# Kernel tuning notes

Hardware: AMD Instinct MI355X
Metric: run time of the kernel (lower is better)

## Reference

```python
import jax, jax.numpy as jnp
import numpy as np

D_MODEL = 512
N_HEADS = 8
D_K = D_MODEL // N_HEADS
WINDOW = 32  # attention restricted to |i-j| <= WINDOW//2
SCALE = float(np.sqrt(D_K))


def setup_inputs() -> dict:
    key = jax.random.key(0)
    ks = jax.random.split(key, 11)
    B, S, D = 2, 4096, D_MODEL
    inv = 1.0 / np.sqrt(D)
    inp = {
        "query": jax.random.normal(ks[0], (B, S, D), jnp.float32),
        "key": jax.random.normal(ks[1], (B, S, D), jnp.float32),
        "value": jax.random.normal(ks[2], (B, S, D), jnp.float32),
        # torch nn.Linear params: weight (out,in), bias (out,)
        "wq": jax.random.uniform(ks[3], (D, D), jnp.float32, -inv, inv),
        "bq": jax.random.uniform(ks[4], (D,), jnp.float32, -inv, inv),
        "wk": jax.random.uniform(ks[5], (D, D), jnp.float32, -inv, inv),
        "bk": jax.random.uniform(ks[6], (D,), jnp.float32, -inv, inv),
        "wv": jax.random.uniform(ks[7], (D, D), jnp.float32, -inv, inv),
        "bv": jax.random.uniform(ks[8], (D,), jnp.float32, -inv, inv),
        "wo": jax.random.uniform(ks[9], (D, D), jnp.float32, -inv, inv),
        "bo": jax.random.uniform(ks[10], (D,), jnp.float32, -inv, inv),
    }
    return inp


def _linear(x, w, b):
    # torch: y = x @ w.T + b
    return jnp.einsum('bsd,od->bso', x, w) + b


def reference(query, key, value, wq, bq, wk, bk, wv, bv, wo, bo):
    B, S, D = query.shape
    # project and split heads -> [B, H, S, d_k]
    def split(x):
        return x.reshape(B, S, N_HEADS, D_K).transpose(0, 2, 1, 3)
    Q = split(_linear(query, wq, bq))
    K = split(_linear(key, wk, bk))
    V = split(_linear(value, wv, bv))
    # full scores then banded mask (faithful to original dense-masked impl)
    scores = jnp.einsum('bhqd,bhkd->bhqk', Q, K) / SCALE
    i = jnp.arange(S)[:, None]
    j = jnp.arange(S)[None, :]
    band = jnp.abs(i - j) <= (WINDOW // 2)  # [S, S]
    scores = jnp.where(band[None, None, :, :], scores, -1e9)
    attn = jax.nn.softmax(scores, axis=-1)
    ctx = jnp.einsum('bhqk,bhkd->bhqd', attn, V)
    ctx = ctx.transpose(0, 2, 1, 3).reshape(B, S, D)
    return _linear(ctx, wo, bo)
```

## Files before the change

kernel.cpp:

```cpp
#include <hip/hip_runtime.h>
#include <hip/hip_bf16.h>

using u16 = unsigned short;
using u32 = unsigned int;

typedef float f32x4 __attribute__((ext_vector_type(4)));
typedef __bf16 bf16x8 __attribute__((ext_vector_type(8)));

constexpr int B_ = 2;
constexpr int S_ = 4096;
constexpr int D_ = 512;
constexpr int H_ = 8;
constexpr int DK_ = 64;
constexpr int M_ = B_ * S_;
constexpr int K_ = 512;

__device__ __forceinline__ float bf2f(u16 u) {
  return __uint_as_float(((u32)u) << 16);
}
__device__ __forceinline__ u16 f2bf(float x) {
  u32 u = __float_as_uint(x);
  u = (u + 0x7fffu + ((u >> 16) & 1u)) >> 16;
  return (u16)u;
}
__device__ __forceinline__ u32 pack2(float a, float b) {
  return (u32)f2bf(a) | ((u32)f2bf(b) << 16);
}
__device__ __forceinline__ u32 cvtpk(float a, float b) {
  u32 r;
  asm("v_cvt_pk_bf16_f32 %0, %1, %2" : "=v"(r) : "v"(a), "v"(b));
  return r;
}

__device__ __forceinline__ void gload16(const void* g, void* l) {
  __builtin_amdgcn_global_load_lds((const __attribute__((address_space(1))) void*)g,
                                   (__attribute__((address_space(3))) void*)l,
                                   16, 0, 0);
}

constexpr int NG_W = 4 * (262144 / 8);

__global__ __launch_bounds__(256) void convert_w(
    const float* __restrict__ wq, const float* __restrict__ wk,
    const float* __restrict__ wv, const float* __restrict__ wo,
    u16* __restrict__ wqb, u16* __restrict__ wkb, u16* __restrict__ wvb,
    u16* __restrict__ wob)
{
  const int g8 = blockIdx.x * 256 + threadIdx.x;
  if (g8 >= NG_W) return;
  const int t = g8 >> 15;
  const int r = g8 & 32767;
  const float* s = (t == 0) ? wq : (t == 1) ? wk : (t == 2) ? wv : wo;
  u16* d = (t == 0) ? wqb : (t == 1) ? wkb : (t == 2) ? wvb : wob;
  const size_t off = (size_t)r * 8;
  const float4 x = *(const float4*)(s + off);
  const float4 y = *(const float4*)(s + off + 4);
  uint4 o;
  o.x = pack2(x.x, x.y); o.y = pack2(x.z, x.w);
  o.z = pack2(y.x, y.y); o.w = pack2(y.z, y.w);
  *(uint4*)(d + off) = o;
}

template<int MODE>
__device__ __forceinline__ void gemm_qkv_body(const float* __restrict__ A,
                                              const u16* __restrict__ Wt,
                                              const float* __restrict__ bias,
                                              void* __restrict__ Cout,
                                              u16* __restrict__ As,
                                              u16* __restrict__ Bs2)
{
  const int tid  = threadIdx.x;
  const int lane = tid & 63;
  const int w    = tid >> 6;
  const int wm   = w >> 1;
  const int wn   = w & 1;
  const int m0   = blockIdx.x * 128;
  const int n0   = blockIdx.y * 128;
  const int qr   = lane & 15;
  const int g    = lane >> 4;

  const int sr8 = tid >> 3;
  const int c8  = tid & 7;
  const float* afp = A + (size_t)(m0 + sr8) * K_ + c8 * 8;
  char* awr = (char*)As + sr8 * 128 + ((c8 ^ (sr8 & 7)) * 16);

  float4 ax_[4], ay_[4];
  auto a_issue = [&](int t) {
#pragma unroll
    for (int p = 0; p < 4; ++p) {
      const float* s = afp + t * 64 + (size_t)(p * 32) * K_;
      ax_[p] = *(const float4*)s;
      ay_[p] = *(const float4*)(s + 4);
    }
  };
  auto a_write = [&]() {
#pragma unroll
    for (int p = 0; p < 4; ++p) {
      uint4 o;
      o.x = cvtpk(ax_[p].x, ax_[p].y);
      o.y = cvtpk(ax_[p].z, ax_[p].w);
      o.z = cvtpk(ay_[p].x, ay_[p].y);
      o.w = cvtpk(ay_[p].z, ay_[p].w);
      *(uint4*)(awr + p * 32 * 128) = o;
    }
  };

  const int swz8 = ((lane & 7) ^ (lane >> 3)) * 8;
  const u16* b0 = Wt + (size_t)(n0 + w * 32 + (lane >> 3)) * K_ + swz8;
  auto stage_B = [&](int t, int buf) {
    u16* dst = Bs2 + buf * (128 * 64) + (w * 32) * 64;
#pragma unroll
    for (int p = 0; p < 4; ++p)
      gload16(b0 + t * 64 + (size_t)p * 8 * K_, dst + (p * 8) * 64);
  };

  f32x4 acc[4][4] = {};

  a_issue(0);
  stage_B(0, 0);
  a_write();
  __syncthreads();

  const int axr = (qr & 7) << 4;
  const char* ab = (const char*)As + (wm * 64 + qr) * 128;

  constexpr int NT = K_ / 64;
#pragma unroll 1
  for (int t = 0; t < NT; ++t) {
    const int buf = t & 1;
    if (t + 1 < NT) {
      a_issue(t + 1);
      stage_B(t + 1, buf ^ 1);
    }

    const char* bb = (const char*)(Bs2 + buf * (128 * 64)) + (wn * 64 + qr) * 128;
#pragma unroll
    for (int kk = 0; kk < 2; ++kk) {
      bf16x8 af[4], bfr[4];
#pragma unroll
      for (int i = 0; i < 4; ++i)
        af[i]  = *(const bf16x8*)(ab + i * 2048 + ((g * 16 + kk * 64) ^ axr));
#pragma unroll
      for (int j = 0; j < 4; ++j)
        bfr[j] = *(const bf16x8*)(bb + j * 2048 + ((g * 16 + kk * 64) ^ axr));
#pragma unroll
      for (int i = 0; i < 4; ++i)
#pragma unroll
        for (int j = 0; j < 4; ++j)
          acc[i][j] = __builtin_amdgcn_mfma_f32_16x16x32_bf16(af[i], bfr[j], acc[i][j], 0, 0, 0);
    }

    if (t + 1 < NT) {
      __syncthreads();
      a_write();
      __syncthreads();
    }
  }

#pragma unroll
  for (int j = 0; j < 4; ++j) {
    const int col = n0 + wn * 64 + j * 16 + qr;
    const float bv = bias[col];
#pragma unroll
    for (int i = 0; i < 4; ++i) {
      const int rbase = m0 + wm * 64 + i * 16 + g * 4;
      if constexpr (MODE == 2) {
        const int bb2 = rbase >> 12;
        const int ss = rbase & (S_ - 1);
        const int hh = col >> 6;
        const int dd = col & (DK_ - 1);
        uint2 pk;
        pk.x = pack2(acc[i][j][0] + bv, acc[i][j][1] + bv);
        pk.y = pack2(acc[i][j][2] + bv, acc[i][j][3] + bv);
        *(uint2*)&((u16*)Cout)[((size_t)((bb2 * H_ + hh) * DK_ + dd)) * S_ + ss] = pk;
      } else {
#pragma unroll
        for (int r = 0; r < 4; ++r)
          ((u16*)Cout)[(size_t)(rbase + r) * D_ + col] = f2bf(acc[i][j][r] + bv);
      }
    }
  }
}

__global__ __launch_bounds__(256, 3) void gemm_qkv(
    const float* __restrict__ q, const float* __restrict__ k, const float* __restrict__ v,
    const u16* __restrict__ wqb, const u16* __restrict__ wkb, const u16* __restrict__ wvb,
    const float* __restrict__ bq, const float* __restrict__ bk, const float* __restrict__ bv,
    u16* __restrict__ Qo, u16* __restrict__ Ko, u16* __restrict__ Vo)
{
  __shared__ u16 As[128 * 64];
  __shared__ u16 Bs2[2][128 * 64];
  if (blockIdx.z == 0)      gemm_qkv_body<0>(q, wqb, bq, Qo, As, &Bs2[0][0]);
  else if (blockIdx.z == 1) gemm_qkv_body<0>(k, wkb, bk, Ko, As, &Bs2[0][0]);
  else                      gemm_qkv_body<2>(v, wvb, bv, Vo, As, &Bs2[0][0]);
}

__global__ __launch_bounds__(256, 2) void gemm_out(
    const u16* __restrict__ A, const u16* __restrict__ Wt,
    const float* __restrict__ bias, float* __restrict__ C)
{
  __shared__ u16 As2[2][64 * 64];
  __shared__ u16 Bs2[2][128 * 64];

  const int tid  = threadIdx.x;
  const int lane = tid & 63;
  const int w    = tid >> 6;
  const int wm   = w >> 1;
  const int wn   = w & 1;
  const int m0   = blockIdx.x * 64;
  const int n0   = blockIdx.y * 128;
  const int qr   = lane & 15;
  const int g    = lane >> 4;

  const int swz8 = ((lane & 7) ^ (lane >> 3)) * 8;
  const u16* a0 = A  + (size_t)(m0 + w * 16 + (lane >> 3)) * K_ + swz8;
  const u16* b0 = Wt + (size_t)(n0 + w * 32 + (lane >> 3)) * K_ + swz8;

  auto stage = [&](int t, int buf) {
#pragma unroll
    for (int p = 0; p < 2; ++p)
      gload16(a0 + t * 64 + (size_t)p * 8 * K_, &As2[buf][(w * 16 + p * 8) * 64]);
#pragma unroll
    for (int p = 0; p < 4; ++p)
      gload16(b0 + t * 64 + (size_t)p * 8 * K_, &Bs2[buf][(w * 32 + p * 8) * 64]);
  };

  f32x4 acc[2][4] = {};
  stage(0, 0);
  __syncthreads();

  const int ax = (qr & 7) << 4;

  constexpr int NT = K_ / 64;
#pragma unroll 1
  for (int t = 0; t < NT; ++t) {
    const int buf = t & 1;
    if (t + 1 < NT) stage(t + 1, buf ^ 1);

    const char* ab = (const char*)&As2[buf][0] + (wm * 32 + qr) * 128;
    const char* bb = (const char*)&Bs2[buf][0] + (wn * 64 + qr) * 128;
#pragma unroll
    for (int kk = 0; kk < 2; ++kk) {
      bf16x8 af[2], bfr[4];
#pragma unroll
      for (int i = 0; i < 2; ++i)
        af[i]  = *(const bf16x8*)(ab + i * 2048 + ((g * 16 + kk * 64) ^ ax));
#pragma unroll
      for (int j = 0; j < 4; ++j)
        bfr[j] = *(const bf16x8*)(bb + j * 2048 + ((g * 16 + kk * 64) ^ ax));
#pragma unroll
      for (int i = 0; i < 2; ++i)
#pragma unroll
        for (int j = 0; j < 4; ++j)
          acc[i][j] = __builtin_amdgcn_mfma_f32_16x16x32_bf16(af[i], bfr[j], acc[i][j], 0, 0, 0);
    }
    if (t + 1 < NT) __syncthreads();
  }

#pragma unroll
  for (int j = 0; j < 4; ++j) {
    const int col = n0 + wn * 64 + j * 16 + qr;
    const float bv = bias[col];
#pragma unroll
    for (int i = 0; i < 2; ++i) {
      const int rbase = m0 + wm * 32 + i * 16 + g * 4;
#pragma unroll
      for (int r = 0; r < 4; ++r)
        C[(size_t)(rbase + r) * D_ + col] = acc[i][j][r] + bv;
    }
  }
}

__global__ __launch_bounds__(256) void attn_band_mfma(
    const u16* __restrict__ Q, const u16* __restrict__ K,
    const u16* __restrict__ Vt, u16* __restrict__ Ctx)
{
  constexpr int LDP = 72;
  __shared__ u16 P_lds[4][16 * LDP];

  const int lane = threadIdx.x & 63;
  const int w    = threadIdx.x >> 6;
  const int wid  = blockIdx.x * 4 + w;
  const int q0   = (wid & 255) << 4;
  const int bh   = wid >> 8;
  const int bb   = bh >> 3;
  const int hh   = bh & (H_ - 1);

  u16* pl = &P_lds[w][0];
  const int qr = lane & 15;
  const int g  = lane >> 4;

  *(uint2*)&pl[qr * LDP + 48 + 4 * g] = make_uint2(0u, 0u);

  bf16x8 qf[2];
  {
    const u16* qp = Q + ((size_t)(bb * S_ + q0 + qr)) * D_ + hh * DK_ + 8 * g;
    qf[0] = *(const bf16x8*)qp;
    qf[1] = *(const bf16x8*)(qp + 32);
  }

  f32x4 sc[3];
#pragma unroll
  for (int t = 0; t < 3; ++t) {
    int j = q0 - 16 + 16 * t + qr;
    j = min(max(j, 0), S_ - 1);
    const u16* kp = K + ((size_t)(bb * S_ + j)) * D_ + hh * DK_ + 8 * g;
    const bf16x8 kf0 = *(const bf16x8*)kp;
    const bf16x8 kf1 = *(const bf16x8*)(kp + 32);
    f32x4 a = {};
    a = __builtin_amdgcn_mfma_f32_16x16x32_bf16(kf0, qf[0], a, 0, 0, 0);
    a = __builtin_amdgcn_mfma_f32_16x16x32_bf16(kf1, qf[1], a, 0, 0, 0);
    sc[t] = a;
  }

  float s[3][4];
  float mx = -INFINITY;
#pragma unroll
  for (int t = 0; t < 3; ++t)
#pragma unroll
    for (int r = 0; r < 4; ++r) {
      const int joff = 16 * t + 4 * g + r;
      const int j = q0 - 16 + joff;
      const bool ok = (joff >= qr) && (joff <= qr + 32) && (j >= 0) && (j < S_);
      const float v = ok ? sc[t][r] * 0.125f : -INFINITY;
      s[t][r] = v;
      mx = fmaxf(mx, v);
    }
  mx = fmaxf(mx, __shfl_xor(mx, 16));
  mx = fmaxf(mx, __shfl_xor(mx, 32));

  float p[3][4];
  float den = 0.f;
#pragma unroll
  for (int t = 0; t < 3; ++t)
#pragma unroll
    for (int r = 0; r < 4; ++r) {
      p[t][r] = __expf(s[t][r] - mx);
      den += p[t][r];
    }
  den += __shfl_xor(den, 16);
  den += __shfl_xor(den, 32);
  const float inv = 1.0f / den;

#pragma unroll
  for (int t = 0; t < 3; ++t) {
    uint2 pk;
    pk.x = pack2(p[t][0] * inv, p[t][1] * inv);
    pk.y = pack2(p[t][2] * inv, p[t][3] * inv);
    *(uint2*)&pl[qr * LDP + 16 * t + 4 * g] = pk;
  }

  f32x4 cacc[4] = {};
#pragma unroll
  for (int jc = 0; jc < 2; ++jc) {
    const bf16x8 pa = *(const bf16x8*)&pl[qr * LDP + 8 * g + 32 * jc];
#pragma unroll
    for (int nt = 0; nt < 4; ++nt) {
      int jj = q0 - 16 + 8 * g + 32 * jc;
      jj = min(max(jj, 0), S_ - 8);
      const u16* vp = Vt + ((size_t)bh * DK_ + 16 * nt + qr) * S_ + jj;
      const bf16x8 vf = *(const bf16x8*)vp;
      cacc[nt] = __builtin_amdgcn_mfma_f32_16x16x32_bf16(pa, vf, cacc[nt], 0, 0, 0);
    }
  }

#pragma unroll
  for (int nt = 0; nt < 4; ++nt)
#pragma unroll
    for (int r = 0; r < 4; ++r) {
      const int qq = 4 * g + r;
      const int dd = 16 * nt + qr;
      Ctx[((size_t)(bb * S_ + q0 + qq)) * D_ + hh * DK_ + dd] = f2bf(cacc[nt][r]);
    }
}

extern "C" void kernel_launch(void* const* d_in, const int* in_sizes, int n_in,
                              void* d_out, int out_size, void* d_ws, size_t ws_size,
                              hipStream_t stream)
{
  const float* query = (const float*)d_in[0];
  const float* key   = (const float*)d_in[1];
  const float* value = (const float*)d_in[2];
  const float* wq    = (const float*)d_in[3];
  const float* bq    = (const float*)d_in[4];
  const float* wk    = (const float*)d_in[5];
  const float* bk    = (const float*)d_in[6];
  const float* wv    = (const float*)d_in[7];
  const float* bv    = (const float*)d_in[8];
  const float* wo    = (const float*)d_in[9];
  const float* bo    = (const float*)d_in[10];

  const size_t seg = (size_t)M_ * D_;
  u16* Qw  = (u16*)d_ws;
  u16* Kw  = Qw + seg;
  u16* Vw  = Kw + seg;
  u16* Cw  = Vw + seg;
  u16* wqb = Cw + seg;
  u16* wkb = wqb + (size_t)D_ * D_;
  u16* wvb = wkb + (size_t)D_ * D_;
  u16* wob = wvb + (size_t)D_ * D_;

  dim3 blk(256);
  convert_w<<<dim3((NG_W + 255) / 256), blk, 0, stream>>>(
      wq, wk, wv, wo, wqb, wkb, wvb, wob);
  gemm_qkv<<<dim3(M_ / 128, D_ / 128, 3), blk, 0, stream>>>(
      query, key, value, wqb, wkb, wvb, bq, bk, bv, Qw, Kw, Vw);
  attn_band_mfma<<<dim3((B_ * H_ * S_) / 64), blk, 0, stream>>>(Qw, Kw, Vw, Cw);
  gemm_out<<<dim3(M_ / 64, D_ / 128), blk, 0, stream>>>(Cw, wob, bo, (float*)d_out);
}
```

Baseline: 55.11 us.

## Fuse weight bf16 conversion into QKV GEMM and attention kernels, drop convert kernel

Removes the separate weight-conversion kernel launch. The QKV GEMM now loads fp32 weights and converts them to bf16 in registers before writing to LDS, and the output-projection weight conversion is folded into the attention kernel's prologue. This saves a launch and a pass over the weights, but doubles weight bytes read per GEMM block, adds conversion ALU work and registers, and replaces the async double-buffered B staging with synchronous single-buffer staging.

```diff
diff --git a/kernel.cpp b/kernel.cpp
--- a/kernel.cpp
+++ b/kernel.cpp
@@ -38,36 +38,13 @@
                                    16, 0, 0);
 }
 
-constexpr int NG_W = 4 * (262144 / 8);
-
-__global__ __launch_bounds__(256) void convert_w(
-    const float* __restrict__ wq, const float* __restrict__ wk,
-    const float* __restrict__ wv, const float* __restrict__ wo,
-    u16* __restrict__ wqb, u16* __restrict__ wkb, u16* __restrict__ wvb,
-    u16* __restrict__ wob)
-{
-  const int g8 = blockIdx.x * 256 + threadIdx.x;
-  if (g8 >= NG_W) return;
-  const int t = g8 >> 15;
-  const int r = g8 & 32767;
-  const float* s = (t == 0) ? wq : (t == 1) ? wk : (t == 2) ? wv : wo;
-  u16* d = (t == 0) ? wqb : (t == 1) ? wkb : (t == 2) ? wvb : wob;
-  const size_t off = (size_t)r * 8;
-  const float4 x = *(const float4*)(s + off);
-  const float4 y = *(const float4*)(s + off + 4);
-  uint4 o;
-  o.x = pack2(x.x, x.y); o.y = pack2(x.z, x.w);
-  o.z = pack2(y.x, y.y); o.w = pack2(y.z, y.w);
-  *(uint4*)(d + off) = o;
-}
-
 template<int MODE>
 __device__ __forceinline__ void gemm_qkv_body(const float* __restrict__ A,
-                                              const u16* __restrict__ Wt,
+                                              const float* __restrict__ W,
                                               const float* __restrict__ bias,
                                               void* __restrict__ Cout,
                                               u16* __restrict__ As,
-                                              u16* __restrict__ Bs2)
+                                              u16* __restrict__ Bs)
 {
   const int tid  = threadIdx.x;
   const int lane = tid & 63;
@@ -81,16 +58,28 @@
 
   const int sr8 = tid >> 3;
   const int c8  = tid & 7;
+  const int swb = (c8 ^ (sr8 & 7)) * 16;
+
   const float* afp = A + (size_t)(m0 + sr8) * K_ + c8 * 8;
-  char* awr = (char*)As + sr8 * 128 + ((c8 ^ (sr8 & 7)) * 16);
-
-  float4 ax_[4], ay_[4];
+  const float* wfp = W + (size_t)(n0 + sr8) * K_ + c8 * 8;
+  char* awr = (char*)As + sr8 * 128 + swb;
+  char* bwr = (char*)Bs + sr8 * 128 + swb;
+
+  float4 ax_[4], ay_[4], bx_[4], by_[4];
   auto a_issue = [&](int t) {
 #pragma unroll
     for (int p = 0; p < 4; ++p) {
       const float* s = afp + t * 64 + (size_t)(p * 32) * K_;
       ax_[p] = *(const float4*)s;
       ay_[p] = *(const float4*)(s + 4);
+    }
+  };
+  auto b_issue = [&](int t) {
+#pragma unroll
+    for (int p = 0; p < 4; ++p) {
+      const float* s = wfp + t * 64 + (size_t)(p * 32) * K_;
+      bx_[p] = *(const float4*)s;
+      by_[p] = *(const float4*)(s + 4);
     }
   };
   auto a_write = [&]() {
@@ -104,36 +93,36 @@
       *(uint4*)(awr + p * 32 * 128) = o;
     }
   };
-
-  const int swz8 = ((lane & 7) ^ (lane >> 3)) * 8;
-  const u16* b0 = Wt + (size_t)(n0 + w * 32 + (lane >> 3)) * K_ + swz8;
-  auto stage_B = [&](int t, int buf) {
-    u16* dst = Bs2 + buf * (128 * 64) + (w * 32) * 64;
-#pragma unroll
-    for (int p = 0; p < 4; ++p)
-      gload16(b0 + t * 64 + (size_t)p * 8 * K_, dst + (p * 8) * 64);
+  auto b_write = [&]() {
+#pragma unroll
+    for (int p = 0; p < 4; ++p) {
+      uint4 o;
+      o.x = cvtpk(bx_[p].x, bx_[p].y);
+      o.y = cvtpk(bx_[p].z, bx_[p].w);
+      o.z = cvtpk(by_[p].x, by_[p].y);
+      o.w = cvtpk(by_[p].z, by_[p].w);
+      *(uint4*)(bwr + p * 32 * 128) = o;
+    }
   };
 
   f32x4 acc[4][4] = {};
 
-  a_issue(0);
-  stage_B(0, 0);
-  a_write();
+  a_issue(0); b_issue(0);
+  a_write(); b_write();
   __syncthreads();
 
   const int axr = (qr & 7) << 4;
   const char* ab = (const char*)As + (wm * 64 + qr) * 128;
+  const char* bb = (const char*)Bs + (wn * 64 + qr) * 128;
 
   constexpr int NT = K_ / 64;
 #pragma unroll 1
   for (int t = 0; t < NT; ++t) {
-    const int buf = t & 1;
     if (t + 1 < NT) {
       a_issue(t + 1);
-      stage_B(t + 1, buf ^ 1);
-    }
-
-    const char* bb = (const char*)(Bs2 + buf * (128 * 64)) + (wn * 64 + qr) * 128;
+      b_issue(t + 1);
+    }
+
 #pragma unroll
     for (int kk = 0; kk < 2; ++kk) {
       bf16x8 af[4], bfr[4];
@@ -153,6 +142,7 @@
     if (t + 1 < NT) {
       __syncthreads();
       a_write();
+      b_write();
       __syncthreads();
     }
   }
@@ -184,15 +174,15 @@
 
 __global__ __launch_bounds__(256, 3) void gemm_qkv(
     const float* __restrict__ q, const float* __restrict__ k, const float* __restrict__ v,
-    const u16* __restrict__ wqb, const u16* __restrict__ wkb, const u16* __restrict__ wvb,
+    const float* __restrict__ wq, const float* __restrict__ wk, const float* __restrict__ wv,
     const float* __restrict__ bq, const float* __restrict__ bk, const float* __restrict__ bv,
     u16* __restrict__ Qo, u16* __restrict__ Ko, u16* __restrict__ Vo)
 {
   __shared__ u16 As[128 * 64];
-  __shared__ u16 Bs2[2][128 * 64];
-  if (blockIdx.z == 0)      gemm_qkv_body<0>(q, wqb, bq, Qo, As, &Bs2[0][0]);
-  else if (blockIdx.z == 1) gemm_qkv_body<0>(k, wkb, bk, Ko, As, &Bs2[0][0]);
-  else                      gemm_qkv_body<2>(v, wvb, bv, Vo, As, &Bs2[0][0]);
+  __shared__ u16 Bs[128 * 64];
+  if (blockIdx.z == 0)      gemm_qkv_body<0>(q, wq, bq, Qo, As, Bs);
+  else if (blockIdx.z == 1) gemm_qkv_body<0>(k, wk, bk, Ko, As, Bs);
+  else                      gemm_qkv_body<2>(v, wv, bv, Vo, As, Bs);
 }
 
 __global__ __launch_bounds__(256, 2) void gemm_out(
@@ -273,8 +263,14 @@
 
 __global__ __launch_bounds__(256) void attn_band_mfma(
     const u16* __restrict__ Q, const u16* __restrict__ K,
-    const u16* __restrict__ Vt, u16* __restrict__ Ctx)
+    const u16* __restrict__ Vt, u16* __restrict__ Ctx,
+    const float* __restrict__ wo, u16* __restrict__ wob)
 {
+  {
+    const int idx = blockIdx.x * 256 + threadIdx.x;
+    wob[idx] = f2bf(wo[idx]);
+  }
+
   constexpr int LDP = 72;
   __shared__ u16 P_lds[4][16 * LDP];
 
@@ -395,16 +391,12 @@
   u16* Kw  = Qw + seg;
   u16* Vw  = Kw + seg;
   u16* Cw  = Vw + seg;
-  u16* wqb = Cw + seg;
-  u16* wkb = wqb + (size_t)D_ * D_;
-  u16* wvb = wkb + (size_t)D_ * D_;
-  u16* wob = wvb + (size_t)D_ * D_;
+  u16* wob = Cw + seg;
 
   dim3 blk(256);
-  convert_w<<<dim3((NG_W + 255) / 256), blk, 0, stream>>>(
-      wq, wk, wv, wo, wqb, wkb, wvb, wob);
   gemm_qkv<<<dim3(M_ / 128, D_ / 128, 3), blk, 0, stream>>>(
-      query, key, value, wqb, wkb, wvb, bq, bk, bv, Qw, Kw, Vw);
-  attn_band_mfma<<<dim3((B_ * H_ * S_) / 64), blk, 0, stream>>>(Qw, Kw, Vw, Cw);
+      query, key, value, wq, wk, wv, bq, bk, bv, Qw, Kw, Vw);
+  attn_band_mfma<<<dim3((B_ * H_ * S_) / 64), blk, 0, stream>>>(
+      Qw, Kw, Vw, Cw, wo, wob);
   gemm_out<<<dim3(M_ / 64, D_ / 128), blk, 0, stream>>>(Cw, wob, bo, (float*)d_out);
 }
```

New measurement: 56.26 us. 2.1% more time.

## Load QKV A-operand directly into MFMA registers; shrink out-proj tile to 32 rows

Applied to the files above, without the earlier changes.

The QKV projection GEMM now reads fp32 activations straight from global memory into the per-lane MFMA fragment layout and converts them to bf16 in registers. This removes the A-tile LDS staging buffer and one barrier per k-step. The cost is uncoalesced, redundant global reads, since each of the two wn warps loads the same A rows. The output GEMM drops from 64-row to 32-row tiles with 4 warps split along N and launch bounds raised to 4 blocks per CU, doubling the grid for better occupancy at lower per-warp MFMA reuse.

```diff
diff --git a/kernel.cpp b/kernel.cpp
--- a/kernel.cpp
+++ b/kernel.cpp
@@ -66,7 +66,6 @@
                                               const u16* __restrict__ Wt,
                                               const float* __restrict__ bias,
                                               void* __restrict__ Cout,
-                                              u16* __restrict__ As,
                                               u16* __restrict__ Bs2)
 {
   const int tid  = threadIdx.x;
@@ -79,30 +78,32 @@
   const int qr   = lane & 15;
   const int g    = lane >> 4;
 
-  const int sr8 = tid >> 3;
-  const int c8  = tid & 7;
-  const float* afp = A + (size_t)(m0 + sr8) * K_ + c8 * 8;
-  char* awr = (char*)As + sr8 * 128 + ((c8 ^ (sr8 & 7)) * 16);
-
-  float4 ax_[4], ay_[4];
+  const float* arow = A + (size_t)(m0 + wm * 64 + qr) * K_ + 8 * g;
+
+  float4 palo[4][2], pahi[4][2];
   auto a_issue = [&](int t) {
 #pragma unroll
-    for (int p = 0; p < 4; ++p) {
-      const float* s = afp + t * 64 + (size_t)(p * 32) * K_;
-      ax_[p] = *(const float4*)s;
-      ay_[p] = *(const float4*)(s + 4);
-    }
+    for (int i = 0; i < 4; ++i)
+#pragma unroll
+      for (int kk = 0; kk < 2; ++kk) {
+        const float* s = arow + (size_t)(i * 16) * K_ + t * 64 + kk * 32;
+        palo[i][kk] = *(const float4*)s;
+        pahi[i][kk] = *(const float4*)(s + 4);
+      }
   };
-  auto a_write = [&]() {
-#pragma unroll
-    for (int p = 0; p < 4; ++p) {
-      uint4 o;
-      o.x = cvtpk(ax_[p].x, ax_[p].y);
-      o.y = cvtpk(ax_[p].z, ax_[p].w);
-      o.z = cvtpk(ay_[p].x, ay_[p].y);
-      o.w = cvtpk(ay_[p].z, ay_[p].w);
-      *(uint4*)(awr + p * 32 * 128) = o;
-    }
+  bf16x8 af[4][2];
+  auto a_cvt = [&]() {
+#pragma unroll
+    for (int i = 0; i < 4; ++i)
+#pragma unroll
+      for (int kk = 0; kk < 2; ++kk) {
+        union { u32 u[4]; bf16x8 v; } u;
+        u.u[0] = cvtpk(palo[i][kk].x, palo[i][kk].y);
+        u.u[1] = cvtpk(palo[i][kk].z, palo[i][kk].w);
+        u.u[2] = cvtpk(pahi[i][kk].x, pahi[i][kk].y);
+        u.u[3] = cvtpk(pahi[i][kk].z, pahi[i][kk].w);
+        af[i][kk] = u.v;
+      }
   };
 
   const int swz8 = ((lane & 7) ^ (lane >> 3)) * 8;
@@ -118,11 +119,10 @@
 
   a_issue(0);
   stage_B(0, 0);
-  a_write();
   __syncthreads();
+  a_cvt();
 
   const int axr = (qr & 7) << 4;
-  const char* ab = (const char*)As + (wm * 64 + qr) * 128;
 
   constexpr int NT = K_ / 64;
 #pragma unroll 1
@@ -136,10 +136,7 @@
     const char* bb = (const char*)(Bs2 + buf * (128 * 64)) + (wn * 64 + qr) * 128;
 #pragma unroll
     for (int kk = 0; kk < 2; ++kk) {
-      bf16x8 af[4], bfr[4];
-#pragma unroll
-      for (int i = 0; i < 4; ++i)
-        af[i]  = *(const bf16x8*)(ab + i * 2048 + ((g * 16 + kk * 64) ^ axr));
+      bf16x8 bfr[4];
 #pragma unroll
       for (int j = 0; j < 4; ++j)
         bfr[j] = *(const bf16x8*)(bb + j * 2048 + ((g * 16 + kk * 64) ^ axr));
@@ -147,13 +144,12 @@
       for (int i = 0; i < 4; ++i)
 #pragma unroll
         for (int j = 0; j < 4; ++j)
-          acc[i][j] = __builtin_amdgcn_mfma_f32_16x16x32_bf16(af[i], bfr[j], acc[i][j], 0, 0, 0);
+          acc[i][j] = __builtin_amdgcn_mfma_f32_16x16x32_bf16(af[i][kk], bfr[j], acc[i][j], 0, 0, 0);
     }
 
     if (t + 1 < NT) {
       __syncthreads();
-      a_write();
-      __syncthreads();
+      a_cvt();
     }
   }
 
@@ -188,44 +184,40 @@
     const float* __restrict__ bq, const float* __restrict__ bk, const float* __restrict__ bv,
     u16* __restrict__ Qo, u16* __restrict__ Ko, u16* __restrict__ Vo)
 {
-  __shared__ u16 As[128 * 64];
   __shared__ u16 Bs2[2][128 * 64];
-  if (blockIdx.z == 0)      gemm_qkv_body<0>(q, wqb, bq, Qo, As, &Bs2[0][0]);
-  else if (blockIdx.z == 1) gemm_qkv_body<0>(k, wkb, bk, Ko, As, &Bs2[0][0]);
-  else                      gemm_qkv_body<2>(v, wvb, bv, Vo, As, &Bs2[0][0]);
-}
-
-__global__ __launch_bounds__(256, 2) void gemm_out(
+  if (blockIdx.z == 0)      gemm_qkv_body<0>(q, wqb, bq, Qo, &Bs2[0][0]);
+  else if (blockIdx.z == 1) gemm_qkv_body<0>(k, wkb, bk, Ko, &Bs2[0][0]);
+  else                      gemm_qkv_body<2>(v, wvb, bv, Vo, &Bs2[0][0]);
+}
+
+__global__ __launch_bounds__(256, 4) void gemm_out(
     const u16* __restrict__ A, const u16* __restrict__ Wt,
     const float* __restrict__ bias, float* __restrict__ C)
 {
-  __shared__ u16 As2[2][64 * 64];
+  __shared__ u16 As2[2][32 * 64];
   __shared__ u16 Bs2[2][128 * 64];
 
   const int tid  = threadIdx.x;
   const int lane = tid & 63;
   const int w    = tid >> 6;
-  const int wm   = w >> 1;
-  const int wn   = w & 1;
-  const int m0   = blockIdx.x * 64;
+  const int wn   = w;
+  const int m0   = blockIdx.x * 32;
   const int n0   = blockIdx.y * 128;
   const int qr   = lane & 15;
   const int g    = lane >> 4;
 
   const int swz8 = ((lane & 7) ^ (lane >> 3)) * 8;
-  const u16* a0 = A  + (size_t)(m0 + w * 16 + (lane >> 3)) * K_ + swz8;
+  const u16* a0 = A  + (size_t)(m0 + w * 8 + (lane >> 3)) * K_ + swz8;
   const u16* b0 = Wt + (size_t)(n0 + w * 32 + (lane >> 3)) * K_ + swz8;
 
   auto stage = [&](int t, int buf) {
-#pragma unroll
-    for (int p = 0; p < 2; ++p)
-      gload16(a0 + t * 64 + (size_t)p * 8 * K_, &As2[buf][(w * 16 + p * 8) * 64]);
+    gload16(a0 + t * 64, &As2[buf][(w * 8) * 64]);
 #pragma unroll
     for (int p = 0; p < 4; ++p)
       gload16(b0 + t * 64 + (size_t)p * 8 * K_, &Bs2[buf][(w * 32 + p * 8) * 64]);
   };
 
-  f32x4 acc[2][4] = {};
+  f32x4 acc[2][2] = {};
   stage(0, 0);
   __syncthreads();
 
@@ -237,33 +229,33 @@
     const int buf = t & 1;
     if (t + 1 < NT) stage(t + 1, buf ^ 1);
 
-    const char* ab = (const char*)&As2[buf][0] + (wm * 32 + qr) * 128;
-    const char* bb = (const char*)&Bs2[buf][0] + (wn * 64 + qr) * 128;
+    const char* ab = (const char*)&As2[buf][0] + qr * 128;
+    const char* bb = (const char*)&Bs2[buf][0] + (wn * 32 + qr) * 128;
 #pragma unroll
     for (int kk = 0; kk < 2; ++kk) {
-      bf16x8 af[2], bfr[4];
+      bf16x8 af[2], bfr[2];
 #pragma unroll
       for (int i = 0; i < 2; ++i)
         af[i]  = *(const bf16x8*)(ab + i * 2048 + ((g * 16 + kk * 64) ^ ax));
 #pragma unroll
-      for (int j = 0; j < 4; ++j)
+      for (int j = 0; j < 2; ++j)
         bfr[j] = *(const bf16x8*)(bb + j * 2048 + ((g * 16 + kk * 64) ^ ax));
 #pragma unroll
       for (int i = 0; i < 2; ++i)
 #pragma unroll
-        for (int j = 0; j < 4; ++j)
+        for (int j = 0; j < 2; ++j)
           acc[i][j] = __builtin_amdgcn_mfma_f32_16x16x32_bf16(af[i], bfr[j], acc[i][j], 0, 0, 0);
     }
     if (t + 1 < NT) __syncthreads();
   }
 
 #pragma unroll
-  for (int j = 0; j < 4; ++j) {
-    const int col = n0 + wn * 64 + j * 16 + qr;
+  for (int j = 0; j < 2; ++j) {
+    const int col = n0 + wn * 32 + j * 16 + qr;
     const float bv = bias[col];
 #pragma unroll
     for (int i = 0; i < 2; ++i) {
-      const int rbase = m0 + wm * 32 + i * 16 + g * 4;
+      const int rbase = m0 + i * 16 + g * 4;
 #pragma unroll
       for (int r = 0; r < 4; ++r)
         C[(size_t)(rbase + r) * D_ + col] = acc[i][j][r] + bv;
@@ -406,5 +398,5 @@
   gemm_qkv<<<dim3(M_ / 128, D_ / 128, 3), blk, 0, stream>>>(
       query, key, value, wqb, wkb, wvb, bq, bk, bv, Qw, Kw, Vw);
   attn_band_mfma<<<dim3((B_ * H_ * S_) / 64), blk, 0, stream>>>(Qw, Kw, Vw, Cw);
-  gemm_out<<<dim3(M_ / 64, D_ / 128), blk, 0, stream>>>(Cw, wob, bo, (float*)d_out);
-}
+  gemm_out<<<dim3(M_ / 32, D_ / 128), blk, 0, stream>>>(Cw, wob, bo, (float*)d_out);
+}
```

After: 109.3 us. +98.4%, slower.
